# Kernel optimization log

Hardware: AMD Instinct MI355X
Metric: run time of the kernel (lower is better)

## Reference

```python
import jax, jax.numpy as jnp
import numpy as np

B, S, E, H = 2, 2048, 1024, 16
DH = E // H


def setup_inputs() -> dict:
    key = jax.random.key(0)
    ks = jax.random.split(key, 8)
    scale = 1.0 / np.sqrt(E)
    return {
        "in_feats": jax.random.normal(ks[0], (B, S, E), jnp.float32),
        "mul_encs": jax.random.normal(ks[1], (B, S, E), jnp.float32),
        "add_encs": jax.random.normal(ks[2], (B, S, E), jnp.float32),
        "ln_w": jnp.ones((E,), jnp.float32),
        "ln_b": jnp.zeros((E,), jnp.float32),
        "in_proj_w": jax.random.uniform(ks[3], (3 * E, E), jnp.float32, -scale, scale),
        "in_proj_b": jnp.zeros((3 * E,), jnp.float32),
        "out_proj_w": jax.random.uniform(ks[4], (E, E), jnp.float32, -scale, scale),
        "out_proj_b": jnp.zeros((E,), jnp.float32),
    }


def _layernorm(x, w, b, eps=1e-5):
    mu = jnp.mean(x, axis=-1, keepdims=True)
    var = jnp.var(x, axis=-1, keepdims=True)
    return (x - mu) * jax.lax.rsqrt(var + eps) * w + b


def reference(in_feats, mul_encs, add_encs, ln_w, ln_b, in_proj_w, in_proj_b, out_proj_w, out_proj_b):
    # norm + act pre-processing (torch nn.GELU default = exact erf gelu)
    d = _layernorm(in_feats, ln_w, ln_b)
    d = jax.nn.gelu(d, approximate=False)
    values = d
    qk_in = d * mul_encs + add_encs  # QK encoding modulation

    wq, wk, wv = jnp.split(in_proj_w, 3, axis=0)
    bq, bk, bv = jnp.split(in_proj_b, 3, axis=0)
    q = (qk_in @ wq.T + bq).reshape(B, S, H, DH)
    k = (qk_in @ wk.T + bk).reshape(B, S, H, DH)
    v = (values @ wv.T + bv).reshape(B, S, H, DH)

    scale = 1.0 / np.sqrt(DH)
    scores = jnp.einsum("bqhd,bkhd->bhqk", q * scale, k)  # [B,H,S,S]
    attn = jax.nn.softmax(scores, axis=-1)
    out = jnp.einsum("bhqk,bkhd->bqhd", attn, v).reshape(B, S, E)
    out = out @ out_proj_w.T + out_proj_b
    return in_feats + out  # skip connection
```

## Files before the change

### kernel.cpp

```cpp
#include <hip/hip_runtime.h>
#include <stdint.h>


typedef __attribute__((ext_vector_type(8))) short bf16x8;
typedef __attribute__((ext_vector_type(4))) short bf16x4;
typedef __attribute__((ext_vector_type(4))) float f32x4;
typedef __attribute__((ext_vector_type(4))) unsigned short u16x4;

#define DEV __device__ __forceinline__

DEV unsigned short f2bf(float f) {
  uint32_t u = __float_as_uint(f);
  u += 0x7fff + ((u >> 16) & 1);
  return (unsigned short)(u >> 16);
}

DEV float fast_exp2(float x) {
#if __has_builtin(__builtin_amdgcn_exp2f)
  return __builtin_amdgcn_exp2f(x);
#else
  return exp2f(x);
#endif
}

DEV f32x4 mfma16x16x16_bf16(bf16x4 a, bf16x4 b, f32x4 c) {
#if __has_builtin(__builtin_amdgcn_mfma_f32_16x16x16bf16_1k)
  return __builtin_amdgcn_mfma_f32_16x16x16bf16_1k(a, b, c, 0, 0, 0);
#else
  asm("v_mfma_f32_16x16x16_bf16 %0, %1, %2, %0" : "+v"(c) : "v"(a), "v"(b));
  return c;
#endif
}

DEV void gload_lds16(const void* g, void* l) {
  __builtin_amdgcn_global_load_lds(
      (const __attribute__((address_space(1))) uint32_t*)g,
      (__attribute__((address_space(3))) uint32_t*)l, 16, 0, 0);
}

__global__ __launch_bounds__(256) void preproc_wconv(const float* x, const float* mul, const float* add,
                                                     const float* lw, const float* lb,
                                                     unsigned short* values, unsigned short* qkin,
                                                     const float* w1, const float* w2,
                                                     unsigned short* o1, unsigned short* o2) {
  int t = threadIdx.x;
  if (blockIdx.x >= 4096) {
    int i = (blockIdx.x - 4096) * 256 + t;
    const int n1 = 3145728 / 4;
    f32x4 v;
    if (i < n1) v = ((const f32x4*)w1)[i];
    else        v = ((const f32x4*)w2)[i - n1];
    u16x4 r;
#pragma unroll
    for (int j = 0; j < 4; ++j) r[j] = f2bf(v[j]);
    if (i < n1) ((u16x4*)o1)[i] = r;
    else        ((u16x4*)o2)[i - n1] = r;
    return;
  }
  int row = blockIdx.x;
  size_t base = (size_t)row * 1024;
  f32x4 v = ((const f32x4*)(x + base))[t];
  float s  = v[0] + v[1] + v[2] + v[3];
  float s2 = v[0]*v[0] + v[1]*v[1] + v[2]*v[2] + v[3]*v[3];
#pragma unroll
  for (int off = 1; off < 64; off <<= 1) {
    s  += __shfl_xor(s, off);
    s2 += __shfl_xor(s2, off);
  }
  __shared__ float rs[4], rs2[4];
  if ((t & 63) == 0) { rs[t >> 6] = s; rs2[t >> 6] = s2; }
  __syncthreads();
  s  = rs[0] + rs[1] + rs[2] + rs[3];
  s2 = rs2[0] + rs2[1] + rs2[2] + rs2[3];
  float mean = s * 0.0009765625f;
  float var  = s2 * 0.0009765625f - mean * mean;
  float rstd = rsqrtf(var + 1e-5f);
  f32x4 mu = ((const f32x4*)(mul + base))[t];
  f32x4 ad = ((const f32x4*)(add + base))[t];
  f32x4 w4 = ((const f32x4*)lw)[t];
  f32x4 b4 = ((const f32x4*)lb)[t];
  u16x4 vo, qo;
#pragma unroll
  for (int i = 0; i < 4; ++i) {
    float d = (v[i] - mean) * rstd * w4[i] + b4[i];
    float g = 0.5f * d * (1.0f + erff(d * 0.70710678118f));
    vo[i] = f2bf(g);
    qo[i] = f2bf(g * mu[i] + ad[i]);
  }
  ((u16x4*)(values + base))[t] = vo;
  ((u16x4*)(qkin   + base))[t] = qo;
}

DEV void gemm_tile(const unsigned short* A, const unsigned short* B, int K,
                   int m0, int n0, unsigned short* ldsA, unsigned short* ldsB,
                   f32x4 acc[4][4]) {
  int t = threadIdx.x;
  int lane = t & 63;
  int w = t >> 6;
  int wr = w >> 1, wc = w & 1;
  int l15 = lane & 15, l4 = lane >> 4;
  for (int k0 = 0; k0 < K; k0 += 64) {
#pragma unroll
    for (int i = 0; i < 4; ++i) {
      int idx = i * 256 + t;
      int r = idx >> 3;
      int slot = (idx & 7) ^ (r & 7);
      gload_lds16(A + (size_t)(m0 + r) * K + k0 + slot * 8,
                  (char*)ldsA + i * 4096 + w * 1024);
      gload_lds16(B + (size_t)(n0 + r) * K + k0 + slot * 8,
                  (char*)ldsB + i * 4096 + w * 1024);
    }
    __syncthreads();
#pragma unroll
    for (int kk = 0; kk < 2; ++kk) {
      bf16x8 af[4], bfr[4];
      int kb = kk * 64 + l4 * 16;
#pragma unroll
      for (int mm = 0; mm < 4; ++mm) {
        int r = wr * 64 + mm * 16 + l15;
        af[mm] = *(const bf16x8*)((const char*)ldsA + r * 128 + (kb ^ ((r & 7) << 4)));
      }
#pragma unroll
      for (int nn = 0; nn < 4; ++nn) {
        int r = wc * 64 + nn * 16 + l15;
        bfr[nn] = *(const bf16x8*)((const char*)ldsB + r * 128 + (kb ^ ((r & 7) << 4)));
      }
#pragma unroll
      for (int mm = 0; mm < 4; ++mm)
#pragma unroll
        for (int nn = 0; nn < 4; ++nn)
          acc[mm][nn] = __builtin_amdgcn_mfma_f32_16x16x32_bf16(af[mm], bfr[nn], acc[mm][nn], 0, 0, 0);
    }
    __syncthreads();
  }
}

#define QSCALE 0.18033688011112042f

__global__ __launch_bounds__(256) void gemm_qkv(const unsigned short* Aqk, const unsigned short* Av,
                                                const unsigned short* W, const float* bias,
                                                unsigned short* qws, unsigned short* kws,
                                                unsigned short* vtws) {
  __shared__ unsigned short lds[2 * 128 * 64];
  unsigned short* ldsA = lds;
  unsigned short* ldsB = lds + 128 * 64;
  int id = blockIdx.x;
  int xcd = id & 7, rr = id >> 3;
  int bx = xcd * 3 + (rr % 3);
  int by = rr / 3;
  int n0 = bx * 128;
  int m0 = by * 128;
  const unsigned short* A = (n0 < 2048) ? Aqk : Av;
  f32x4 z = {0.f, 0.f, 0.f, 0.f};
  f32x4 acc[4][4];
#pragma unroll
  for (int mm = 0; mm < 4; ++mm)
#pragma unroll
    for (int nn = 0; nn < 4; ++nn) acc[mm][nn] = z;
  gemm_tile(A, W, 1024, m0, n0, ldsA, ldsB, acc);

  int t = threadIdx.x, lane = t & 63, w = t >> 6;
  int wr = w >> 1, wc = w & 1;
  int l15 = lane & 15, l4 = lane >> 4;
  int region = n0 >> 10;
  int bb = m0 >> 11, s0 = m0 & 2047;

  if (region == 2) {
    __syncthreads();
#pragma unroll
    for (int mm = 0; mm < 4; ++mm) {
#pragma unroll
      for (int nn = 0; nn < 4; ++nn) {
        int col = wc * 64 + nn * 16 + l15;
        float bs = bias[n0 + col];
#pragma unroll
        for (int reg = 0; reg < 4; ++reg) {
          int row = wr * 64 + mm * 16 + l4 * 4 + reg;
          *(unsigned short*)((char*)lds + row * 256 + ((col * 2) ^ ((row & 7) << 4))) =
              f2bf(acc[mm][nn][reg] + bs);
        }
      }
    }
    __syncthreads();
    int c = t >> 1, hl = t & 1;
    int e0 = n0 - 2048;
    int h = (e0 + c) >> 6, d = (e0 + c) & 63;
    unsigned short* dst = vtws + ((size_t)(bb * 16 + h) * 64 + d) * 2048 + s0 + hl * 64;
#pragma unroll
    for (int j0 = 0; j0 < 64; j0 += 8) {
      bf16x8 pk;
#pragma unroll
      for (int j = 0; j < 8; ++j) {
        int s = hl * 64 + j0 + j;
        pk[j] = *(const short*)((const char*)lds + s * 256 + ((c * 2) ^ ((s & 7) << 4)));
      }
      *(bf16x8*)(dst + j0) = pk;
    }
  } else {
    unsigned short* dst0 = region == 0 ? qws : kws;
    float scl = region == 0 ? QSCALE : 1.0f;
#pragma unroll
    for (int mm = 0; mm < 4; ++mm) {
      int row0 = m0 + wr * 64 + mm * 16 + l4 * 4;
      int sr = row0 & 2047;
#pragma unroll
      for (int nn = 0; nn < 4; ++nn) {
        int col = n0 + wc * 64 + nn * 16 + l15;
        float bs = bias[col];
        int e = col & 1023;
        int h = e >> 6, d = e & 63;
#pragma unroll
        for (int reg = 0; reg < 4; ++reg)
          dst0[(((size_t)(bb * 16 + h)) * 2048 + sr + reg) * 64 + d] = f2bf((acc[mm][nn][reg] + bs) * scl);
      }
    }
  }
}

DEV void stage_k(const unsigned short* Kp, int kv0, unsigned short* buf, int t) {
  int w = t >> 6;
#pragma unroll
  for (int i = 0; i < 2; ++i) {
    int idx = i * 256 + t;
    int r = idx >> 3;
    int slot = (idx & 7) ^ (r & 7);
    gload_lds16(Kp + (size_t)(kv0 + r) * 64 + slot * 8,
                (char*)buf + i * 4096 + w * 1024);
  }
}

DEV void stage_vt(const unsigned short* Vt, int kv0, unsigned short* buf, int t) {
  int w = t >> 6;
#pragma unroll
  for (int i = 0; i < 2; ++i) {
    int idx = i * 256 + t;
    int r = idx >> 3;
    int slot = (idx & 7) ^ (r & 7);
    gload_lds16(Vt + (size_t)r * 2048 + kv0 + slot * 8,
                (char*)buf + i * 4096 + w * 1024);
  }
}

DEV void attn_compute(const unsigned short* kbuf, const unsigned short* vtbuf,
                      const bf16x8 (&aq)[2][2], f32x4 (&o)[2][4],
                      float (&m_run)[2], float (&l_run)[2], const int (&osrc)[4],
                      int l15, int l4) {
  f32x4 z = {0.f, 0.f, 0.f, 0.f};
  f32x4 sc[2][4];
#pragma unroll
  for (int qs = 0; qs < 2; ++qs)
#pragma unroll
    for (int nn = 0; nn < 4; ++nn) sc[qs][nn] = z;
  __builtin_amdgcn_s_setprio(1);
#pragma unroll
  for (int kk = 0; kk < 2; ++kk) {
#pragma unroll
    for (int nn = 0; nn < 4; ++nn) {
      int r = nn * 16 + l15;
      bf16x8 bk = *(const bf16x8*)((const char*)kbuf + r * 128 + ((kk * 64 + l4 * 16) ^ ((r & 7) << 4)));
#pragma unroll
      for (int qs = 0; qs < 2; ++qs)
        sc[qs][nn] = __builtin_amdgcn_mfma_f32_16x16x32_bf16(bk, aq[qs][kk], sc[qs][nn], 0, 0, 0);
    }
  }
  __builtin_amdgcn_s_setprio(0);

  bf16x4 pa[2][4];
  float pmax[2];
#pragma unroll
  for (int qs = 0; qs < 2; ++qs) {
    float mA = fmaxf(fmaxf(sc[qs][0][0], sc[qs][0][1]), fmaxf(sc[qs][0][2], sc[qs][0][3]));
    float mB = fmaxf(fmaxf(sc[qs][1][0], sc[qs][1][1]), fmaxf(sc[qs][1][2], sc[qs][1][3]));
    float mC = fmaxf(fmaxf(sc[qs][2][0], sc[qs][2][1]), fmaxf(sc[qs][2][2], sc[qs][2][3]));
    float mD = fmaxf(fmaxf(sc[qs][3][0], sc[qs][3][1]), fmaxf(sc[qs][3][2], sc[qs][3][3]));
    float pm = fmaxf(fmaxf(mA, mB), fmaxf(mC, mD));
    pm = fmaxf(pm, __shfl_xor(pm, 16));
    pm = fmaxf(pm, __shfl_xor(pm, 32));
    pmax[qs] = pm;
  }

  if (__any(fmaxf(pmax[0] - m_run[0], pmax[1] - m_run[1]) > 8.0f)) {
#pragma unroll
    for (int qs = 0; qs < 2; ++qs) {
      float mnew = fmaxf(m_run[qs], pmax[qs]);
      float fs = fast_exp2(m_run[qs] - mnew);
      m_run[qs] = mnew;
      l_run[qs] *= fs;
      float fo[4];
#pragma unroll
      for (int reg = 0; reg < 4; ++reg) fo[reg] = __shfl(fs, osrc[reg]);
#pragma unroll
      for (int dt = 0; dt < 4; ++dt)
#pragma unroll
        for (int reg = 0; reg < 4; ++reg) o[qs][dt][reg] *= fo[reg];
    }
  }

#pragma unroll
  for (int qs = 0; qs < 2; ++qs) {
    float psum = 0.f;
#pragma unroll
    for (int nn = 0; nn < 4; ++nn) {
      float p0 = fast_exp2(sc[qs][nn][0] - m_run[qs]);
      float p1 = fast_exp2(sc[qs][nn][1] - m_run[qs]);
      float p2 = fast_exp2(sc[qs][nn][2] - m_run[qs]);
      float p3 = fast_exp2(sc[qs][nn][3] - m_run[qs]);
      psum += (p0 + p1) + (p2 + p3);
      pa[qs][nn][0] = (short)(__float_as_uint(p0) >> 16);
      pa[qs][nn][1] = (short)(__float_as_uint(p1) >> 16);
      pa[qs][nn][2] = (short)(__float_as_uint(p2) >> 16);
      pa[qs][nn][3] = (short)(__float_as_uint(p3) >> 16);
    }
    psum += __shfl_xor(psum, 16);
    psum += __shfl_xor(psum, 32);
    l_run[qs] += psum;
  }

  __builtin_amdgcn_s_setprio(1);
#pragma unroll
  for (int dt = 0; dt < 4; ++dt) {
    int r = dt * 16 + l15;
#pragma unroll
    for (int nn = 0; nn < 4; ++nn) {
      bf16x4 vb = *(const bf16x4*)((const char*)vtbuf + r * 128 + ((nn * 32 + l4 * 8) ^ ((r & 7) << 4)));
#pragma unroll
      for (int qs = 0; qs < 2; ++qs)
        o[qs][dt] = mfma16x16x16_bf16(pa[qs][nn], vb, o[qs][dt]);
    }
  }
  __builtin_amdgcn_s_setprio(0);
}

__global__ __launch_bounds__(256, 4) void attn_kernel(const unsigned short* qws, const unsigned short* kws,
                                                      const unsigned short* vtws,
                                                      unsigned short* po0, unsigned short* po1,
                                                      float* stats) {
  int id = blockIdx.x;
  int xcd = id & 7, rr = id >> 3;
  int c = xcd * 8 + (rr & 7);
  int qt = rr >> 3;
  int bh = c & 31;
  int half = c >> 5;
  int q0 = qt * 128;
  int kvbase = half * 1024;
  int t = threadIdx.x;
  int lane = t & 63, w = t >> 6;
  int l15 = lane & 15, l4 = lane >> 4;
  __shared__ unsigned short ldsK[2][64 * 64];
  __shared__ unsigned short ldsVT[2][64 * 64];

  const unsigned short* Qp = qws + ((size_t)bh * 2048 + q0 + w * 32) * 64;
  const unsigned short* Kp = kws + ((size_t)bh * 2048 + kvbase) * 64;
  const unsigned short* Vt = vtws + (size_t)bh * 64 * 2048 + kvbase;

  bf16x8 aq[2][2];
#pragma unroll
  for (int qs = 0; qs < 2; ++qs)
#pragma unroll
    for (int kk = 0; kk < 2; ++kk)
      aq[qs][kk] = *(const bf16x8*)(Qp + (qs * 16 + l15) * 64 + kk * 32 + l4 * 8);

  f32x4 z = {0.f, 0.f, 0.f, 0.f};
  f32x4 o[2][4];
#pragma unroll
  for (int qs = 0; qs < 2; ++qs)
#pragma unroll
    for (int i = 0; i < 4; ++i) o[qs][i] = z;
  float m_run[2] = {-1e30f, -1e30f};
  float l_run[2] = {0.f, 0.f};

  int osrc[4];
#pragma unroll
  for (int reg = 0; reg < 4; ++reg)
    osrc[reg] = (lane & 48) | (((lane >> 4) & 3) << 2) | reg;

  stage_k(Kp, 0, &ldsK[0][0], t);
  stage_vt(Vt, 0, &ldsVT[0][0], t);
  __syncthreads();

  for (int it = 0; it < 16; ++it) {
    int cur = it & 1;
    if (it < 15) {
      stage_k(Kp, (it + 1) * 64, &ldsK[cur ^ 1][0], t);
      stage_vt(Vt, (it + 1) * 64, &ldsVT[cur ^ 1][0], t);
    }
    attn_compute(&ldsK[cur][0], &ldsVT[cur][0], aq, o, m_run, l_run, osrc, l15, l4);
    __syncthreads();
  }

  unsigned short* po = half ? po1 : po0;
#pragma unroll
  for (int qs = 0; qs < 2; ++qs) {
#pragma unroll
    for (int reg = 0; reg < 4; ++reg) {
      int qg = q0 + w * 32 + qs * 16 + l4 * 4 + reg;
#pragma unroll
      for (int dt = 0; dt < 4; ++dt) {
        int d = dt * 16 + l15;
        po[((size_t)bh * 2048 + qg) * 64 + d] = f2bf(o[qs][dt][reg]);
      }
    }
  }
  if (l4 == 0) {
#pragma unroll
    for (int qs = 0; qs < 2; ++qs) {
      int qg = q0 + w * 32 + qs * 16 + l15;
      size_t si = (((size_t)half * 32 + bh) * 2048 + qg) * 2;
      stats[si] = m_run[qs];
      stats[si + 1] = l_run[qs];
    }
  }
}

__global__ __launch_bounds__(256) void attn_merge(const unsigned short* po0, const unsigned short* po1,
                                                  const float* stats, unsigned short* attnb) {
  int row = blockIdx.x;
  int b = row >> 11, q = row & 2047;
  int t = threadIdx.x;
  int c0 = t * 4;
  int h = c0 >> 6, d = c0 & 63;
  int bh = b * 16 + h;
  size_t si0 = ((size_t)bh * 2048 + q) * 2;
  size_t si1 = (((size_t)32 + bh) * 2048 + q) * 2;
  float m0 = stats[si0], l0 = stats[si0 + 1];
  float m1 = stats[si1], l1 = stats[si1 + 1];
  float m = fmaxf(m0, m1);
  float f0 = fast_exp2(m0 - m), f1 = fast_exp2(m1 - m);
  float inv = 1.0f / (l0 * f0 + l1 * f1);
  float a0 = f0 * inv, a1 = f1 * inv;
  size_t off = ((size_t)bh * 2048 + q) * 64 + d;
  u16x4 x0 = *(const u16x4*)(po0 + off);
  u16x4 x1 = *(const u16x4*)(po1 + off);
  u16x4 r;
#pragma unroll
  for (int j = 0; j < 4; ++j) {
    float v0 = __uint_as_float((uint32_t)x0[j] << 16);
    float v1 = __uint_as_float((uint32_t)x1[j] << 16);
    r[j] = f2bf(v0 * a0 + v1 * a1);
  }
  *(u16x4*)(attnb + (size_t)row * 1024 + c0) = r;
}

__global__ __launch_bounds__(256) void gemm_out(const unsigned short* A, const unsigned short* W,
                                                const float* bias, const float* resid, float* out) {
  __shared__ unsigned short ldsA[128 * 64];
  __shared__ unsigned short ldsB[64 * 64];
  int id = blockIdx.x;
  int xcd = id & 7, rr = id >> 3;
  int bx = xcd * 2 + (rr & 1);
  int by = rr >> 1;
  int n0 = bx * 64;
  int m0 = by * 128;
  int t = threadIdx.x;
  int lane = t & 63;
  int w = t >> 6;
  int l15 = lane & 15, l4 = lane >> 4;
  f32x4 z = {0.f, 0.f, 0.f, 0.f};
  f32x4 acc[2][4];
#pragma unroll
  for (int mm = 0; mm < 2; ++mm)
#pragma unroll
    for (int nn = 0; nn < 4; ++nn) acc[mm][nn] = z;

  for (int k0 = 0; k0 < 1024; k0 += 64) {
#pragma unroll
    for (int i = 0; i < 4; ++i) {
      int idx = i * 256 + t;
      int r = idx >> 3;
      int slot = (idx & 7) ^ (r & 7);
      gload_lds16(A + (size_t)(m0 + r) * 1024 + k0 + slot * 8,
                  (char*)ldsA + i * 4096 + w * 1024);
    }
#pragma unroll
    for (int i = 0; i < 2; ++i) {
      int idx = i * 256 + t;
      int r = idx >> 3;
      int slot = (idx & 7) ^ (r & 7);
      gload_lds16(W + (size_t)(n0 + r) * 1024 + k0 + slot * 8,
                  (char*)ldsB + i * 4096 + w * 1024);
    }
    __syncthreads();
#pragma unroll
    for (int kk = 0; kk < 2; ++kk) {
      bf16x8 af[2], bfr[4];
      int kb = kk * 64 + l4 * 16;
#pragma unroll
      for (int mm = 0; mm < 2; ++mm) {
        int r = w * 32 + mm * 16 + l15;
        af[mm] = *(const bf16x8*)((const char*)ldsA + r * 128 + (kb ^ ((r & 7) << 4)));
      }
#pragma unroll
      for (int nn = 0; nn < 4; ++nn) {
        int r = nn * 16 + l15;
        bfr[nn] = *(const bf16x8*)((const char*)ldsB + r * 128 + (kb ^ ((r & 7) << 4)));
      }
#pragma unroll
      for (int mm = 0; mm < 2; ++mm)
#pragma unroll
        for (int nn = 0; nn < 4; ++nn)
          acc[mm][nn] = __builtin_amdgcn_mfma_f32_16x16x32_bf16(af[mm], bfr[nn], acc[mm][nn], 0, 0, 0);
    }
    __syncthreads();
  }

#pragma unroll
  for (int mm = 0; mm < 2; ++mm) {
#pragma unroll
    for (int nn = 0; nn < 4; ++nn) {
      int col = n0 + nn * 16 + l15;
      float bs = bias[col];
#pragma unroll
      for (int reg = 0; reg < 4; ++reg) {
        int r = m0 + w * 32 + mm * 16 + l4 * 4 + reg;
        size_t off = (size_t)r * 1024 + col;
        out[off] = acc[mm][nn][reg] + bs + resid[off];
      }
    }
  }
}

extern "C" void kernel_launch(void* const* d_in, const int* in_sizes, int n_in,
                              void* d_out, int out_size, void* d_ws, size_t ws_size,
                              hipStream_t stream) {
  const float* in_feats   = (const float*)d_in[0];
  const float* mul_encs   = (const float*)d_in[1];
  const float* add_encs   = (const float*)d_in[2];
  const float* ln_w       = (const float*)d_in[3];
  const float* ln_b       = (const float*)d_in[4];
  const float* in_proj_w  = (const float*)d_in[5];
  const float* in_proj_b  = (const float*)d_in[6];
  const float* out_proj_w = (const float*)d_in[7];
  const float* out_proj_b = (const float*)d_in[8];
  float* out = (float*)d_out;

  unsigned short* ws = (unsigned short*)d_ws;
  unsigned short* values = ws;
  unsigned short* qkin   = values + 4194304;
  unsigned short* wqkv   = qkin + 4194304;
  unsigned short* wout   = wqkv + 3145728;
  unsigned short* qws    = wout + 1048576;
  unsigned short* kws    = qws + 4194304;
  unsigned short* vtws   = kws + 4194304;
  unsigned short* attnb  = vtws + 4194304;

  unsigned short* po0   = values;
  unsigned short* po1   = qkin;
  float*          stats = (float*)wqkv;

  preproc_wconv<<<8192, 256, 0, stream>>>(in_feats, mul_encs, add_encs, ln_w, ln_b,
                                          values, qkin, in_proj_w, out_proj_w, wqkv, wout);
  gemm_qkv<<<768, 256, 0, stream>>>(qkin, values, wqkv, in_proj_b, qws, kws, vtws);
  attn_kernel<<<1024, 256, 0, stream>>>(qws, kws, vtws, po0, po1, stats);
  attn_merge<<<4096, 256, 0, stream>>>(po0, po1, stats, attnb);
  gemm_out<<<512, 256, 0, stream>>>(attnb, wout, out_proj_b, in_feats, out);
}
```

Baseline: 149.7 us.

## Shrink QKV GEMM M-tile to 64 and compute softmax row sums via MFMA

The QKV projection GEMM now uses 64x128 tiles instead of 128x128 and launches twice as many blocks. This gives more parallelism across CUs and less LDS per block, at the cost of reloading each weight tile more often. In attention, the per-row probability sum is now accumulated with an MFMA against a vector of ones instead of VALU adds and cross-lane shuffles. The row-sum stats are written from a different lane layout to match. The MFMA path also sums the bf16-truncated probabilities, so the sum now matches the values used in P·V.

```diff
diff --git a/kernel.cpp b/kernel.cpp
--- a/kernel.cpp
+++ b/kernel.cpp
@@ -91,91 +91,87 @@
   ((u16x4*)(qkin   + base))[t] = qo;
 }
 
-DEV void gemm_tile(const unsigned short* A, const unsigned short* B, int K,
-                   int m0, int n0, unsigned short* ldsA, unsigned short* ldsB,
-                   f32x4 acc[4][4]) {
-  int t = threadIdx.x;
-  int lane = t & 63;
-  int w = t >> 6;
-  int wr = w >> 1, wc = w & 1;
-  int l15 = lane & 15, l4 = lane >> 4;
-  for (int k0 = 0; k0 < K; k0 += 64) {
-#pragma unroll
-    for (int i = 0; i < 4; ++i) {
-      int idx = i * 256 + t;
-      int r = idx >> 3;
-      int slot = (idx & 7) ^ (r & 7);
-      gload_lds16(A + (size_t)(m0 + r) * K + k0 + slot * 8,
-                  (char*)ldsA + i * 4096 + w * 1024);
-      gload_lds16(B + (size_t)(n0 + r) * K + k0 + slot * 8,
-                  (char*)ldsB + i * 4096 + w * 1024);
-    }
-    __syncthreads();
-#pragma unroll
-    for (int kk = 0; kk < 2; ++kk) {
-      bf16x8 af[4], bfr[4];
-      int kb = kk * 64 + l4 * 16;
-#pragma unroll
-      for (int mm = 0; mm < 4; ++mm) {
-        int r = wr * 64 + mm * 16 + l15;
-        af[mm] = *(const bf16x8*)((const char*)ldsA + r * 128 + (kb ^ ((r & 7) << 4)));
-      }
-#pragma unroll
-      for (int nn = 0; nn < 4; ++nn) {
-        int r = wc * 64 + nn * 16 + l15;
-        bfr[nn] = *(const bf16x8*)((const char*)ldsB + r * 128 + (kb ^ ((r & 7) << 4)));
-      }
-#pragma unroll
-      for (int mm = 0; mm < 4; ++mm)
-#pragma unroll
-        for (int nn = 0; nn < 4; ++nn)
-          acc[mm][nn] = __builtin_amdgcn_mfma_f32_16x16x32_bf16(af[mm], bfr[nn], acc[mm][nn], 0, 0, 0);
-    }
-    __syncthreads();
-  }
-}
-
 #define QSCALE 0.18033688011112042f
 
 __global__ __launch_bounds__(256) void gemm_qkv(const unsigned short* Aqk, const unsigned short* Av,
                                                 const unsigned short* W, const float* bias,
                                                 unsigned short* qws, unsigned short* kws,
                                                 unsigned short* vtws) {
-  __shared__ unsigned short lds[2 * 128 * 64];
+  __shared__ unsigned short lds[(64 + 128) * 64];
   unsigned short* ldsA = lds;
-  unsigned short* ldsB = lds + 128 * 64;
+  unsigned short* ldsB = lds + 64 * 64;
   int id = blockIdx.x;
   int xcd = id & 7, rr = id >> 3;
   int bx = xcd * 3 + (rr % 3);
   int by = rr / 3;
   int n0 = bx * 128;
-  int m0 = by * 128;
+  int m0 = by * 64;
   const unsigned short* A = (n0 < 2048) ? Aqk : Av;
-  f32x4 z = {0.f, 0.f, 0.f, 0.f};
-  f32x4 acc[4][4];
-#pragma unroll
-  for (int mm = 0; mm < 4; ++mm)
-#pragma unroll
-    for (int nn = 0; nn < 4; ++nn) acc[mm][nn] = z;
-  gemm_tile(A, W, 1024, m0, n0, ldsA, ldsB, acc);
-
   int t = threadIdx.x, lane = t & 63, w = t >> 6;
   int wr = w >> 1, wc = w & 1;
   int l15 = lane & 15, l4 = lane >> 4;
+  f32x4 z = {0.f, 0.f, 0.f, 0.f};
+  f32x4 acc[2][4];
+#pragma unroll
+  for (int mm = 0; mm < 2; ++mm)
+#pragma unroll
+    for (int nn = 0; nn < 4; ++nn) acc[mm][nn] = z;
+
+  for (int k0 = 0; k0 < 1024; k0 += 64) {
+#pragma unroll
+    for (int i = 0; i < 2; ++i) {
+      int idx = i * 256 + t;
+      int r = idx >> 3;
+      int slot = (idx & 7) ^ (r & 7);
+      gload_lds16(A + (size_t)(m0 + r) * 1024 + k0 + slot * 8,
+                  (char*)ldsA + i * 4096 + w * 1024);
+    }
+#pragma unroll
+    for (int i = 0; i < 4; ++i) {
+      int idx = i * 256 + t;
+      int r = idx >> 3;
+      int slot = (idx & 7) ^ (r & 7);
+      gload_lds16(W + (size_t)(n0 + r) * 1024 + k0 + slot * 8,
+                  (char*)ldsB + i * 4096 + w * 1024);
+    }
+    __syncthreads();
+#pragma unroll
+    for (int kk = 0; kk < 2; ++kk) {
+      bf16x8 af[2], bfr[4];
+      int kb = kk * 64 + l4 * 16;
+#pragma unroll
+      for (int mm = 0; mm < 2; ++mm) {
+        int r = wr * 32 + mm * 16 + l15;
+        af[mm] = *(const bf16x8*)((const char*)ldsA + r * 128 + (kb ^ ((r & 7) << 4)));
+      }
+#pragma unroll
+      for (int nn = 0; nn < 4; ++nn) {
+        int r = wc * 64 + nn * 16 + l15;
+        bfr[nn] = *(const bf16x8*)((const char*)ldsB + r * 128 + (kb ^ ((r & 7) << 4)));
+      }
+#pragma unroll
+      for (int mm = 0; mm < 2; ++mm)
+#pragma unroll
+        for (int nn = 0; nn < 4; ++nn)
+          acc[mm][nn] = __builtin_amdgcn_mfma_f32_16x16x32_bf16(af[mm], bfr[nn], acc[mm][nn], 0, 0, 0);
+    }
+    __syncthreads();
+  }
+
   int region = n0 >> 10;
   int bb = m0 >> 11, s0 = m0 & 2047;
 
   if (region == 2) {
     __syncthreads();
 #pragma unroll
-    for (int mm = 0; mm < 4; ++mm) {
+    for (int mm = 0; mm < 2; ++mm) {
 #pragma unroll
       for (int nn = 0; nn < 4; ++nn) {
         int col = wc * 64 + nn * 16 + l15;
         float bs = bias[n0 + col];
 #pragma unroll
         for (int reg = 0; reg < 4; ++reg) {
-          int row = wr * 64 + mm * 16 + l4 * 4 + reg;
+          int row = wr * 32 + mm * 16 + l4 * 4 + reg;
           *(unsigned short*)((char*)lds + row * 256 + ((col * 2) ^ ((row & 7) << 4))) =
               f2bf(acc[mm][nn][reg] + bs);
         }
@@ -185,13 +181,13 @@
     int c = t >> 1, hl = t & 1;
     int e0 = n0 - 2048;
     int h = (e0 + c) >> 6, d = (e0 + c) & 63;
-    unsigned short* dst = vtws + ((size_t)(bb * 16 + h) * 64 + d) * 2048 + s0 + hl * 64;
-#pragma unroll
-    for (int j0 = 0; j0 < 64; j0 += 8) {
+    unsigned short* dst = vtws + ((size_t)(bb * 16 + h) * 64 + d) * 2048 + s0 + hl * 32;
+#pragma unroll
+    for (int j0 = 0; j0 < 32; j0 += 8) {
       bf16x8 pk;
 #pragma unroll
       for (int j = 0; j < 8; ++j) {
-        int s = hl * 64 + j0 + j;
+        int s = hl * 32 + j0 + j;
         pk[j] = *(const short*)((const char*)lds + s * 256 + ((c * 2) ^ ((s & 7) << 4)));
       }
       *(bf16x8*)(dst + j0) = pk;
@@ -200,8 +196,8 @@
     unsigned short* dst0 = region == 0 ? qws : kws;
     float scl = region == 0 ? QSCALE : 1.0f;
 #pragma unroll
-    for (int mm = 0; mm < 4; ++mm) {
-      int row0 = m0 + wr * 64 + mm * 16 + l4 * 4;
+    for (int mm = 0; mm < 2; ++mm) {
+      int row0 = m0 + wr * 32 + mm * 16 + l4 * 4;
       int sr = row0 & 2047;
 #pragma unroll
       for (int nn = 0; nn < 4; ++nn) {
@@ -243,8 +239,9 @@
 
 DEV void attn_compute(const unsigned short* kbuf, const unsigned short* vtbuf,
                       const bf16x8 (&aq)[2][2], f32x4 (&o)[2][4],
-                      float (&m_run)[2], float (&l_run)[2], const int (&osrc)[4],
+                      float (&m_run)[2], f32x4 (&l_run4)[2], const int (&osrc)[4],
                       int l15, int l4) {
+  const bf16x4 ones4 = {(short)0x3F80, (short)0x3F80, (short)0x3F80, (short)0x3F80};
   f32x4 z = {0.f, 0.f, 0.f, 0.f};
   f32x4 sc[2][4];
 #pragma unroll
@@ -285,11 +282,12 @@
       float mnew = fmaxf(m_run[qs], pmax[qs]);
       float fs = fast_exp2(m_run[qs] - mnew);
       m_run[qs] = mnew;
-      l_run[qs] *= fs;
       float fo[4];
 #pragma unroll
       for (int reg = 0; reg < 4; ++reg) fo[reg] = __shfl(fs, osrc[reg]);
 #pragma unroll
+      for (int reg = 0; reg < 4; ++reg) l_run4[qs][reg] *= fo[reg];
+#pragma unroll
       for (int dt = 0; dt < 4; ++dt)
 #pragma unroll
         for (int reg = 0; reg < 4; ++reg) o[qs][dt][reg] *= fo[reg];
@@ -298,25 +296,25 @@
 
 #pragma unroll
   for (int qs = 0; qs < 2; ++qs) {
-    float psum = 0.f;
 #pragma unroll
     for (int nn = 0; nn < 4; ++nn) {
       float p0 = fast_exp2(sc[qs][nn][0] - m_run[qs]);
       float p1 = fast_exp2(sc[qs][nn][1] - m_run[qs]);
       float p2 = fast_exp2(sc[qs][nn][2] - m_run[qs]);
       float p3 = fast_exp2(sc[qs][nn][3] - m_run[qs]);
-      psum += (p0 + p1) + (p2 + p3);
       pa[qs][nn][0] = (short)(__float_as_uint(p0) >> 16);
       pa[qs][nn][1] = (short)(__float_as_uint(p1) >> 16);
       pa[qs][nn][2] = (short)(__float_as_uint(p2) >> 16);
       pa[qs][nn][3] = (short)(__float_as_uint(p3) >> 16);
     }
-    psum += __shfl_xor(psum, 16);
-    psum += __shfl_xor(psum, 32);
-    l_run[qs] += psum;
   }
 
   __builtin_amdgcn_s_setprio(1);
+#pragma unroll
+  for (int nn = 0; nn < 4; ++nn)
+#pragma unroll
+    for (int qs = 0; qs < 2; ++qs)
+      l_run4[qs] = mfma16x16x16_bf16(pa[qs][nn], ones4, l_run4[qs]);
 #pragma unroll
   for (int dt = 0; dt < 4; ++dt) {
     int r = dt * 16 + l15;
@@ -367,7 +365,7 @@
 #pragma unroll
     for (int i = 0; i < 4; ++i) o[qs][i] = z;
   float m_run[2] = {-1e30f, -1e30f};
-  float l_run[2] = {0.f, 0.f};
+  f32x4 l_run4[2] = {z, z};
 
   int osrc[4];
 #pragma unroll
@@ -384,7 +382,7 @@
       stage_k(Kp, (it + 1) * 64, &ldsK[cur ^ 1][0], t);
       stage_vt(Vt, (it + 1) * 64, &ldsVT[cur ^ 1][0], t);
     }
-    attn_compute(&ldsK[cur][0], &ldsVT[cur][0], aq, o, m_run, l_run, osrc, l15, l4);
+    attn_compute(&ldsK[cur][0], &ldsVT[cur][0], aq, o, m_run, l_run4, osrc, l15, l4);
     __syncthreads();
   }
 
@@ -407,7 +405,17 @@
       int qg = q0 + w * 32 + qs * 16 + l15;
       size_t si = (((size_t)half * 32 + bh) * 2048 + qg) * 2;
       stats[si] = m_run[qs];
-      stats[si + 1] = l_run[qs];
+    }
+  }
+  if (l15 == 0) {
+#pragma unroll
+    for (int qs = 0; qs < 2; ++qs) {
+#pragma unroll
+      for (int reg = 0; reg < 4; ++reg) {
+        int qg = q0 + w * 32 + qs * 16 + l4 * 4 + reg;
+        size_t si = (((size_t)half * 32 + bh) * 2048 + qg) * 2;
+        stats[si + 1] = l_run4[qs][reg];
+      }
     }
   }
 }
@@ -549,7 +557,7 @@
 
   preproc_wconv<<<8192, 256, 0, stream>>>(in_feats, mul_encs, add_encs, ln_w, ln_b,
                                           values, qkin, in_proj_w, out_proj_w, wqkv, wout);
-  gemm_qkv<<<768, 256, 0, stream>>>(qkin, values, wqkv, in_proj_b, qws, kws, vtws);
+  gemm_qkv<<<1536, 256, 0, stream>>>(qkin, values, wqkv, in_proj_b, qws, kws, vtws);
   attn_kernel<<<1024, 256, 0, stream>>>(qws, kws, vtws, po0, po1, stats);
   attn_merge<<<4096, 256, 0, stream>>>(po0, po1, stats, attnb);
   gemm_out<<<512, 256, 0, stream>>>(attnb, wout, out_proj_b, in_feats, out);
```

Result: faster. 135.6 us (-9.4%).
